# Kernel tuning notes

Hardware: AMD Instinct MI355X
Metric: run time of the kernel (lower is better)

The kernel has to match this reference:

```python
import jax, jax.numpy as jnp
import numpy as np

B, S, D_MODEL, N_HEADS, HIDDEN = 4, 2048, 1024, 16, 4096
D_HEAD = D_MODEL // N_HEADS
LN_EPS = 1e-5


def setup_inputs() -> dict:
    key = jax.random.key(0)
    ks = jax.random.split(key, 20)
    s = 0.02
    return {
        "X": jax.random.normal(ks[0], (B, S, D_MODEL), dtype=jnp.float32),
        # attention projections (stored [in, out]; y = x @ W + b)
        "Wq": jax.random.normal(ks[1], (D_MODEL, D_MODEL), dtype=jnp.float32) * s,
        "bq": jnp.zeros((D_MODEL,), jnp.float32),
        "Wk": jax.random.normal(ks[2], (D_MODEL, D_MODEL), dtype=jnp.float32) * s,
        "bk": jnp.zeros((D_MODEL,), jnp.float32),
        "Wv": jax.random.normal(ks[3], (D_MODEL, D_MODEL), dtype=jnp.float32) * s,
        "bv": jnp.zeros((D_MODEL,), jnp.float32),
        "Wo": jax.random.normal(ks[4], (D_MODEL, D_MODEL), dtype=jnp.float32) * s,
        "bo": jnp.zeros((D_MODEL,), jnp.float32),
        # layernorm 1
        "g1": jnp.ones((D_MODEL,), jnp.float32),
        "beta1": jnp.zeros((D_MODEL,), jnp.float32),
        # FFN
        "W1": jax.random.normal(ks[5], (D_MODEL, HIDDEN), dtype=jnp.float32) * s,
        "b1": jnp.zeros((HIDDEN,), jnp.float32),
        "W2": jax.random.normal(ks[6], (HIDDEN, D_MODEL), dtype=jnp.float32) * s,
        "b2": jnp.zeros((D_MODEL,), jnp.float32),
        # layernorm 2
        "g2": jnp.ones((D_MODEL,), jnp.float32),
        "beta2": jnp.zeros((D_MODEL,), jnp.float32),
    }


def _layer_norm(x, gamma, beta):
    mu = jnp.mean(x, axis=-1, keepdims=True)
    var = jnp.mean(jnp.square(x - mu), axis=-1, keepdims=True)
    return (x - mu) * jax.lax.rsqrt(var + LN_EPS) * gamma + beta


def reference(X, Wq, bq, Wk, bk, Wv, bv, Wo, bo, g1, beta1, W1, b1, W2, b2, g2, beta2):
    b, s, d = X.shape
    # multi-head attention (dropout is identity in eval mode)
    q = (X @ Wq + bq).reshape(b, s, N_HEADS, D_HEAD)
    k = (X @ Wk + bk).reshape(b, s, N_HEADS, D_HEAD)
    v = (X @ Wv + bv).reshape(b, s, N_HEADS, D_HEAD)
    scale = 1.0 / np.sqrt(D_HEAD).astype(np.float32)
    scores = jnp.einsum('bqhd,bkhd->bhqk', q, k) * scale
    attn = jax.nn.softmax(scores, axis=-1)
    ctx = jnp.einsum('bhqk,bkhd->bqhd', attn, v).reshape(b, s, d)
    attn_out = ctx @ Wo + bo
    # AddNorm 1
    Y = _layer_norm(X + attn_out, g1, beta1)
    # FFN
    ffn_out = jax.nn.relu(Y @ W1 + b1) @ W2 + b2
    # AddNorm 2
    return _layer_norm(Y + ffn_out, g2, beta2)
```

## Files before the change

### kernel.cpp

```cpp
#include <hip/hip_runtime.h>
#include <stdint.h>

typedef unsigned short u16;
typedef short bf16x8 __attribute__((ext_vector_type(8)));
typedef float f32x4 __attribute__((ext_vector_type(4)));
typedef float f32x16 __attribute__((ext_vector_type(16)));
typedef u16 u16x4 __attribute__((ext_vector_type(4)));
typedef u16 u16x8 __attribute__((ext_vector_type(8)));

#define LOG2E 1.4426950408889634f
#define QSCALE (0.125f * LOG2E)

__device__ __forceinline__ u16 f2bf(float f) {
  union { float f; uint32_t u; } x; x.f = f;
  uint32_t r = x.u + 0x7fffu + ((x.u >> 16) & 1u);
  return (u16)(r >> 16);
}
__device__ __forceinline__ u16 f2bf_ru(float f) {
  union { float f; uint32_t u; } x; x.f = f;
  return (u16)((x.u + 0x8000u) >> 16);
}
__device__ __forceinline__ float bf2f(u16 h) {
  union { uint32_t u; float f; } x; x.u = ((uint32_t)h) << 16;
  return x.f;
}
__device__ __forceinline__ uint32_t cvtpk(float lo, float hi) {
  uint32_t r;
  asm("v_cvt_pk_bf16_f32 %0, %1, %2" : "=v"(r) : "v"(lo), "v"(hi));
  return r;
}
__device__ __forceinline__ int swz3(int row) { return (row ^ (row >> 3)) & 7; }

__device__ __forceinline__ void gload_lds16(const void* g, void* lds) {
  __builtin_amdgcn_global_load_lds(
      (const __attribute__((address_space(1))) void*)g,
      (__attribute__((address_space(3))) void*)lds, 16, 0, 0);
}

__global__ __launch_bounds__(256) void cast_bf16(const float* __restrict__ in,
                                                 u16* __restrict__ out, int n8) {
  int i = blockIdx.x * 256 + threadIdx.x;
  const int stride = gridDim.x * 256;
  for (; i < n8; i += stride) {
    const f32x4* p = (const f32x4*)in + (size_t)i * 2;
    f32x4 a = p[0], b = p[1];
    u16x8 o;
    o[0] = f2bf(a[0]); o[1] = f2bf(a[1]); o[2] = f2bf(a[2]); o[3] = f2bf(a[3]);
    o[4] = f2bf(b[0]); o[5] = f2bf(b[1]); o[6] = f2bf(b[2]); o[7] = f2bf(b[3]);
    ((u16x8*)out)[i] = o;
  }
}

__global__ __launch_bounds__(256) void concat3(const float* __restrict__ a,
                                               const float* __restrict__ b,
                                               const float* __restrict__ c,
                                               float* __restrict__ o) {
  int i = blockIdx.x * 256 + threadIdx.x;
  if (i < 3072)
    o[i] = i < 1024 ? a[i] * QSCALE : (i < 2048 ? b[i - 1024] : c[i - 2048]);
}

__global__ __launch_bounds__(256) void transpose_cast(const float* __restrict__ in,
                                                      u16* __restrict__ out, int R, int C,
                                                      float scale) {
  __shared__ float tile[32][33];
  const int bc = blockIdx.x * 32, br = blockIdx.y * 32;
  const int tx = threadIdx.x & 31, ty = threadIdx.x >> 5;
#pragma unroll
  for (int i = 0; i < 32; i += 8)
    tile[ty + i][tx] = in[(size_t)(br + ty + i) * C + bc + tx];
  __syncthreads();
#pragma unroll
  for (int i = 0; i < 32; i += 8)
    out[(size_t)(bc + ty + i) * R + br + tx] = f2bf(tile[tx][ty + i] * scale);
}

__global__ __launch_bounds__(256) void vtrans(const u16* __restrict__ QKV,
                                              u16* __restrict__ Vtg) {
  __shared__ u16 tl[64][65];
  const int t = threadIdx.x;
  const int sblk = blockIdx.x, h = blockIdx.y, b = blockIdx.z;
  const int s0 = sblk * 64;
  const size_t ibase = ((size_t)b * 2048) * 3072 + 2048 + h * 64;
#pragma unroll
  for (int i = 0; i < 2; i++) {
    const int idx = i * 256 + t;
    const int sl = idx >> 3, d0 = (idx & 7) * 8;
    bf16x8 v = *(const bf16x8*)&QKV[ibase + (size_t)(s0 + sl) * 3072 + d0];
#pragma unroll
    for (int e = 0; e < 8; e++) tl[d0 + e][sl] = (u16)v[e];
  }
  __syncthreads();
  const size_t ob = ((size_t)(b * 16 + h) * 64) * 2048;
#pragma unroll
  for (int i = 0; i < 2; i++) {
    const int idx = i * 256 + t;
    const int r = idx >> 3, c0 = (idx & 7) * 8;
    u16x8 o;
#pragma unroll
    for (int e = 0; e < 8; e++) o[e] = tl[r][c0 + e];
    *(u16x8*)&Vtg[ob + (size_t)r * 2048 + s0 + c0] = o;
  }
}

template <int RELU>
__global__ __launch_bounds__(256) void gemm_bt(const u16* __restrict__ A,
                                               const u16* __restrict__ BT,
                                               const float* __restrict__ bias,
                                               u16* __restrict__ Cb,
                                               int M, int N, int K) {
  constexpr int BM = 128, BN = 128, BK = 64;
  __shared__ u16 As[BM * BK];
  __shared__ u16 Bs[BN * BK];
  const int t = threadIdx.x;
  const int w = t >> 6, lane = t & 63;
  const int la = lane & 15, lb = lane >> 4;
  const int wr = w >> 1, wc = w & 1;
  const int m0 = blockIdx.y * BM, n0 = blockIdx.x * BN;

  f32x4 acc[4][4];
#pragma unroll
  for (int i = 0; i < 4; i++)
#pragma unroll
    for (int j = 0; j < 4; j++) acc[i][j] = (f32x4){0.f, 0.f, 0.f, 0.f};

  for (int kt = 0; kt < K; kt += BK) {
#pragma unroll
    for (int i = 0; i < 4; i++) {
      const int s = i * 256 + t;
      const int row = s >> 3, col = (s & 7) * 8;
      gload_lds16(A + (size_t)(m0 + row) * K + kt + col, &As[(i * 256 + w * 64) * 8]);
      gload_lds16(BT + (size_t)(n0 + row) * K + kt + col, &Bs[(i * 256 + w * 64) * 8]);
    }
    __syncthreads();
#pragma unroll
    for (int ks = 0; ks < 2; ks++) {
      bf16x8 af[4], bfr[4];
#pragma unroll
      for (int i = 0; i < 4; i++)
        af[i] = *(const bf16x8*)&As[(wr * 64 + i * 16 + la) * BK + ks * 32 + lb * 8];
#pragma unroll
      for (int j = 0; j < 4; j++)
        bfr[j] = *(const bf16x8*)&Bs[(wc * 64 + j * 16 + la) * BK + ks * 32 + lb * 8];
#pragma unroll
      for (int i = 0; i < 4; i++)
#pragma unroll
        for (int j = 0; j < 4; j++)
          acc[i][j] = __builtin_amdgcn_mfma_f32_16x16x32_bf16(af[i], bfr[j], acc[i][j], 0, 0, 0);
    }
    __syncthreads();
  }
#pragma unroll
  for (int i = 0; i < 4; i++) {
    const int r = m0 + wr * 64 + i * 16 + lb * 4;
#pragma unroll
    for (int j = 0; j < 4; j++) {
      const int c = n0 + wc * 64 + j * 16 + la;
      const float bv = bias[c];
#pragma unroll
      for (int rr = 0; rr < 4; rr++) {
        float v = acc[i][j][rr] + bv;
        if (RELU) v = fmaxf(v, 0.f);
        Cb[(size_t)(r + rr) * N + c] = f2bf(v);
      }
    }
  }
}

template <int RELU>
__global__ __launch_bounds__(512, 2) void gemm8p(const u16* __restrict__ A,
                                                 const u16* __restrict__ BT,
                                                 const float* __restrict__ bias,
                                                 u16* __restrict__ Cb,
                                                 int M, int N, int K, int nbx) {
  __shared__ u16 As[2][256 * 64];
  __shared__ u16 Bs[2][256 * 64];
  const int t = threadIdx.x;
  const int w = t >> 6, lane = t & 63;
  const int la = lane & 15, lb = lane >> 4;
  const int wr = w >> 2, wc = w & 3;
  int bid = (int)blockIdx.x;
  const int cpx = (int)gridDim.x >> 3;
  bid = (bid & 7) * cpx + (bid >> 3);
  const int m0 = (bid / nbx) * 256, n0 = (bid % nbx) * 256;
  const int NT = K >> 6;
  const int row64 = t >> 3;
  const int colp = ((t & 7) ^ swz3(row64)) << 3;

#define STG_A(buf, tile, q) \
  gload_lds16(A + (size_t)(m0 + (q)*64 + row64) * K + ((tile) << 6) + colp, \
              &As[buf][(q)*4096 + w * 512])
#define STG_B(buf, tile, q) \
  gload_lds16(BT + (size_t)(n0 + (q)*64 + row64) * K + ((tile) << 6) + colp, \
              &Bs[buf][(q)*4096 + w * 512])
#define LDA(dst, mf, ks) { const int r_ = wr * 128 + (mf)*16 + la; \
  dst = *(const bf16x8*)&As[cur][r_ * 64 + (((((ks) << 2) + lb) ^ swz3(r_)) << 3)]; }
#define LDB(dst, nf, ks) { const int r_ = wc * 64 + (nf)*16 + la; \
  dst = *(const bf16x8*)&Bs[cur][r_ * 64 + (((((ks) << 2) + lb) ^ swz3(r_)) << 3)]; }
#define MFMA16(mh, nh, barr) \
  __builtin_amdgcn_s_setprio(1); \
  _Pragma("unroll") for (int ks = 0; ks < 2; ks++) \
  _Pragma("unroll") for (int i = 0; i < 4; i++) \
  _Pragma("unroll") for (int j = 0; j < 2; j++) \
    acc[(mh)*4 + i][(nh)*2 + j] = __builtin_amdgcn_mfma_f32_16x16x32_bf16( \
        af[i][ks], barr[j][ks], acc[(mh)*4 + i][(nh)*2 + j], 0, 0, 0); \
  __builtin_amdgcn_s_setprio(0);
#define BAR1() __builtin_amdgcn_s_barrier(); \
  asm volatile("s_waitcnt lgkmcnt(0)" ::: "memory"); \
  __builtin_amdgcn_sched_barrier(0)

  f32x4 acc[8][4];
#pragma unroll
  for (int i = 0; i < 8; i++)
#pragma unroll
    for (int j = 0; j < 4; j++) acc[i][j] = (f32x4){0.f, 0.f, 0.f, 0.f};

  STG_A(0, 0, 0); STG_A(0, 0, 2);
  STG_B(0, 0, 0); STG_B(0, 0, 1); STG_B(0, 0, 2); STG_B(0, 0, 3);
  STG_A(0, 0, 1); STG_A(0, 0, 3);
  asm volatile("s_waitcnt vmcnt(2)" ::: "memory");
  __builtin_amdgcn_s_barrier();

  for (int tile = 0; tile < NT; ++tile) {
    const int cur = tile & 1, nxt = cur ^ 1;
    const bool hn = (tile + 1) < NT;
    bf16x8 af[4][2], b0[2][2], b1[2][2];
#pragma unroll
    for (int i = 0; i < 4; i++) { LDA(af[i][0], i, 0); LDA(af[i][1], i, 1); }
#pragma unroll
    for (int j = 0; j < 2; j++) { LDB(b0[j][0], j, 0); LDB(b0[j][1], j, 1); }
    if (hn) { STG_A(nxt, tile + 1, 0); STG_A(nxt, tile + 1, 2); }
    BAR1();
    MFMA16(0, 0, b0);
    __builtin_amdgcn_s_barrier();
#pragma unroll
    for (int j = 0; j < 2; j++) { LDB(b1[j][0], 2 + j, 0); LDB(b1[j][1], 2 + j, 1); }
    if (hn) { STG_B(nxt, tile + 1, 0); STG_B(nxt, tile + 1, 1); }
    BAR1();
    MFMA16(0, 1, b1);
    if (hn) { asm volatile("s_waitcnt vmcnt(4)" ::: "memory"); }
    else    { asm volatile("s_waitcnt vmcnt(0)" ::: "memory"); }
    __builtin_amdgcn_s_barrier();
#pragma unroll
    for (int i = 0; i < 4; i++) { LDA(af[i][0], 4 + i, 0); LDA(af[i][1], 4 + i, 1); }
    if (hn) { STG_B(nxt, tile + 1, 2); STG_B(nxt, tile + 1, 3); }
    BAR1();
    MFMA16(1, 0, b0);
    __builtin_amdgcn_s_barrier();
    if (hn) { STG_A(nxt, tile + 1, 1); STG_A(nxt, tile + 1, 3); }
    BAR1();
    MFMA16(1, 1, b1);
    if (hn) { asm volatile("s_waitcnt vmcnt(2)" ::: "memory"); }
    __builtin_amdgcn_s_barrier();
  }
#undef STG_A
#undef STG_B
#undef LDA
#undef LDB
#undef MFMA16
#undef BAR1

#pragma unroll
  for (int mf = 0; mf < 8; mf++) {
    const int r = m0 + wr * 128 + mf * 16 + lb * 4;
#pragma unroll
    for (int nf = 0; nf < 4; nf++) {
      const int c = n0 + wc * 64 + nf * 16 + la;
      const float bv = bias[c];
#pragma unroll
      for (int rr = 0; rr < 4; rr++) {
        float v = acc[mf][nf][rr] + bv;
        if (RELU) v = fmaxf(v, 0.f);
        Cb[(size_t)(r + rr) * N + c] = f2bf(v);
      }
    }
  }
}

template <int RELU>
__global__ __launch_bounds__(512, 2) void gemm8n(const u16* __restrict__ A,
                                                 const u16* __restrict__ BT,
                                                 const float* __restrict__ bias,
                                                 u16* __restrict__ Cb,
                                                 int M, int N, int K, int nbx) {
  __shared__ u16 As[2][128 * 64];
  __shared__ u16 Bs[2][256 * 64];
  const int t = threadIdx.x;
  const int w = t >> 6, lane = t & 63;
  const int la = lane & 15, lb = lane >> 4;
  const int wr = w >> 2, wc = w & 3;
  int bid = (int)blockIdx.x;
  const int cpx = (int)gridDim.x >> 3;
  bid = (bid & 7) * cpx + (bid >> 3);
  const int m0 = (bid / nbx) * 128, n0 = (bid % nbx) * 256;
  const int NT = K >> 6;
  const int rowA = t >> 3;
  const int colpA = ((t & 7) ^ swz3(rowA)) << 3;

#define STG_An(buf, tile, q) \
  gload_lds16(A + (size_t)(m0 + (q)*64 + rowA) * K + ((tile) << 6) + colpA, \
              &As[buf][(q)*4096 + t * 8])
#define STG_Bn(buf, tile, c, i) { \
  const int r32_ = (i)*64 + (t >> 3); \
  const int R_ = ((r32_ >> 5) << 6) + (c)*32 + (r32_ & 31); \
  const int cp_ = ((t & 7) ^ swz3(R_)) << 3; \
  gload_lds16(BT + (size_t)(n0 + R_) * K + ((tile) << 6) + cp_, \
              &Bs[buf][R_ * 64 + (t & 7) * 8]); }
#define LDAn(dst, mf, ks) { const int r_ = wr * 64 + (mf)*16 + la; \
  dst = *(const bf16x8*)&As[cur][r_ * 64 + (((((ks) << 2) + lb) ^ swz3(r_)) << 3)]; }
#define LDBn(dst, nf, ks) { const int r_ = wc * 64 + (nf)*16 + la; \
  dst = *(const bf16x8*)&Bs[cur][r_ * 64 + (((((ks) << 2) + lb) ^ swz3(r_)) << 3)]; }
#define MFMAn(nh, barr) \
  __builtin_amdgcn_s_setprio(1); \
  _Pragma("unroll") for (int ks = 0; ks < 2; ks++) \
  _Pragma("unroll") for (int i = 0; i < 4; i++) \
  _Pragma("unroll") for (int j = 0; j < 2; j++) \
    acc[i][(nh)*2 + j] = __builtin_amdgcn_mfma_f32_16x16x32_bf16( \
        af[i][ks], barr[j][ks], acc[i][(nh)*2 + j], 0, 0, 0); \
  __builtin_amdgcn_s_setprio(0);
#define BARn() __builtin_amdgcn_s_barrier(); \
  asm volatile("s_waitcnt lgkmcnt(0)" ::: "memory"); \
  __builtin_amdgcn_sched_barrier(0)

  f32x4 acc[4][4];
#pragma unroll
  for (int i = 0; i < 4; i++)
#pragma unroll
    for (int j = 0; j < 4; j++) acc[i][j] = (f32x4){0.f, 0.f, 0.f, 0.f};

  STG_Bn(0, 0, 0, 0); STG_Bn(0, 0, 0, 1); STG_An(0, 0, 0);
  STG_An(0, 0, 1); STG_Bn(0, 0, 1, 0); STG_Bn(0, 0, 1, 1);
  asm volatile("s_waitcnt vmcnt(0)" ::: "memory");
  __builtin_amdgcn_s_barrier();

  for (int tile = 0; tile < NT; ++tile) {
    const int cur = tile & 1, nxt = cur ^ 1;
    const bool hn = (tile + 1) < NT;
    bf16x8 af[4][2], b0[2][2], b1[2][2];
#pragma unroll
    for (int i = 0; i < 4; i++) { LDAn(af[i][0], i, 0); LDAn(af[i][1], i, 1); }
#pragma unroll
    for (int j = 0; j < 2; j++) { LDBn(b0[j][0], j, 0); LDBn(b0[j][1], j, 1); }
    if (hn) { STG_Bn(nxt, tile + 1, 0, 0); STG_Bn(nxt, tile + 1, 0, 1); STG_An(nxt, tile + 1, 0); }
    BARn();
    MFMAn(0, b0);
    if (hn) { asm volatile("s_waitcnt vmcnt(3)" ::: "memory"); }
    else    { asm volatile("s_waitcnt vmcnt(0)" ::: "memory"); }
    __builtin_amdgcn_s_barrier();
#pragma unroll
    for (int j = 0; j < 2; j++) { LDBn(b1[j][0], 2 + j, 0); LDBn(b1[j][1], 2 + j, 1); }
    if (hn) { STG_An(nxt, tile + 1, 1); STG_Bn(nxt, tile + 1, 1, 0); STG_Bn(nxt, tile + 1, 1, 1); }
    BARn();
    MFMAn(1, b1);
    if (hn) { asm volatile("s_waitcnt vmcnt(2)" ::: "memory"); }
    __builtin_amdgcn_s_barrier();
  }
#undef STG_An
#undef STG_Bn
#undef LDAn
#undef LDBn
#undef MFMAn
#undef BARn

#pragma unroll
  for (int mf = 0; mf < 4; mf++) {
    const int r = m0 + wr * 64 + mf * 16 + lb * 4;
#pragma unroll
    for (int nf = 0; nf < 4; nf++) {
      const int c = n0 + wc * 64 + nf * 16 + la;
      const float bv = bias[c];
#pragma unroll
      for (int rr = 0; rr < 4; rr++) {
        float v = acc[mf][nf][rr] + bv;
        if (RELU) v = fmaxf(v, 0.f);
        Cb[(size_t)(r + rr) * N + c] = f2bf(v);
      }
    }
  }
}

__global__ __launch_bounds__(256, 3) void attn_fwd(const u16* __restrict__ Qg,
                                                   const u16* __restrict__ Kg,
                                                   const u16* __restrict__ Vtg,
                                                   u16* __restrict__ Og, int LDM) {
  constexpr int S = 2048, DMO = 1024, NT = S / 64;
  __shared__ u16 Ks[2][64 * 64];
  __shared__ u16 Vt[2][64 * 64];
  const int t = threadIdx.x, w = t >> 6, lane = t & 63;
  const int l5 = lane & 31, hf = lane >> 5;
  const int qb = blockIdx.x, h = blockIdx.y, b = blockIdx.z;
  const size_t base = ((size_t)b * S) * LDM + h * 64;
  const size_t vbase = ((size_t)(b * 16 + h) * 64) * 2048;
  const size_t obase = ((size_t)b * S) * DMO + h * 64;
  const int qrow0 = qb * 128 + w * 32;

#define ATT_STAGE(buf, kt_) { \
  _Pragma("unroll") for (int i = 0; i < 2; i++) { \
    const int s = i * 256 + t; const int r = s >> 3; const int cg = s & 7; \
    gload_lds16(Kg + base + (size_t)((kt_) + r) * LDM + ((cg ^ swz3(r)) << 3), \
                &Ks[buf][s * 8]); } \
  _Pragma("unroll") for (int i = 0; i < 2; i++) { \
    const int s = i * 256 + t; const int r = s >> 3; const int cg = s & 7; \
    gload_lds16(Vtg + vbase + (size_t)r * 2048 + (kt_) + ((cg ^ swz3(r)) << 3), \
                &Vt[buf][s * 8]); } }

  bf16x8 qf[4];
#pragma unroll
  for (int kb = 0; kb < 4; kb++)
    qf[kb] = *(const bf16x8*)&Qg[base + (size_t)(qrow0 + l5) * LDM + kb * 16 + hf * 8];

  f32x16 accO0, accO1, accL;
#pragma unroll
  for (int i = 0; i < 16; i++) { accO0[i] = 0.f; accO1[i] = 0.f; accL[i] = 0.f; }
  float m = -1e30f;

  bf16x8 ones;
#pragma unroll
  for (int i = 0; i < 8; i++) ones[i] = (short)0x3F80;

  ATT_STAGE(0, 0);
  asm volatile("s_waitcnt vmcnt(0)" ::: "memory");
  __builtin_amdgcn_s_barrier();

  for (int kt = 0; kt < NT; ++kt) {
    const int cur = kt & 1;
    if (kt + 1 < NT) ATT_STAGE(cur ^ 1, (kt + 1) * 64);

    f32x16 st0, st1;
#pragma unroll
    for (int i = 0; i < 16; i++) { st0[i] = 0.f; st1[i] = 0.f; }
    __builtin_amdgcn_s_setprio(1);
#pragma unroll
    for (int kb = 0; kb < 4; kb++) {
      const int r0 = l5, r1 = 32 + l5;
      bf16x8 kf0 = *(const bf16x8*)&Ks[cur][r0 * 64 + (((hf + 2 * kb) ^ swz3(r0)) << 3)];
      bf16x8 kf1 = *(const bf16x8*)&Ks[cur][r1 * 64 + (((hf + 2 * kb) ^ swz3(r1)) << 3)];
      st0 = __builtin_amdgcn_mfma_f32_32x32x16_bf16(kf0, qf[kb], st0, 0, 0, 0);
      st1 = __builtin_amdgcn_mfma_f32_32x32x16_bf16(kf1, qf[kb], st1, 0, 0, 0);
    }
    __builtin_amdgcn_s_setprio(0);

    float rm = st0[0];
#pragma unroll
    for (int i = 1; i < 16; i++) rm = fmaxf(rm, st0[i]);
#pragma unroll
    for (int i = 0; i < 16; i++) rm = fmaxf(rm, st1[i]);
    if (__any(rm > m + 8.0f)) {
      float ra = rm, rb = rm;
      asm volatile("v_permlane32_swap_b32 %0, %1" : "+v"(ra), "+v"(rb));
      rm = fmaxf(rm, fmaxf(ra, rb));
      const float mN = fmaxf(m, rm);
      const float al = exp2f(m - mN);
      m = mN;
#pragma unroll
      for (int r = 0; r < 16; r++) {
        const float alr = __shfl(al, (r & 3) + 8 * (r >> 2) + 4 * hf, 64);
        accO0[r] *= alr; accO1[r] *= alr; accL[r] *= alr;
      }
    }

    uint32_t pw0[8], pw1[8];
#pragma unroll
    for (int r2 = 0; r2 < 8; r2++) {
      pw0[r2] = cvtpk(exp2f(st0[2 * r2] - m), exp2f(st0[2 * r2 + 1] - m));
      pw1[r2] = cvtpk(exp2f(st1[2 * r2] - m), exp2f(st1[2 * r2 + 1] - m));
    }
    bf16x8 pf[4];
    {
      uint32_t a0 = pw0[0], b0v = pw0[2], a1 = pw0[1], b1v = pw0[3];
      asm volatile("v_permlane32_swap_b32 %0, %1" : "+v"(a0), "+v"(b0v));
      asm volatile("v_permlane32_swap_b32 %0, %1" : "+v"(a1), "+v"(b1v));
      union { uint32_t u[4]; bf16x8 v; } k;
      k.u[0] = a0; k.u[1] = a1; k.u[2] = b0v; k.u[3] = b1v; pf[0] = k.v;
      uint32_t c0 = pw0[4], d0 = pw0[6], c1 = pw0[5], d1 = pw0[7];
      asm volatile("v_permlane32_swap_b32 %0, %1" : "+v"(c0), "+v"(d0));
      asm volatile("v_permlane32_swap_b32 %0, %1" : "+v"(c1), "+v"(d1));
      k.u[0] = c0; k.u[1] = c1; k.u[2] = d0; k.u[3] = d1; pf[1] = k.v;
      uint32_t e0 = pw1[0], f0 = pw1[2], e1 = pw1[1], f1 = pw1[3];
      asm volatile("v_permlane32_swap_b32 %0, %1" : "+v"(e0), "+v"(f0));
      asm volatile("v_permlane32_swap_b32 %0, %1" : "+v"(e1), "+v"(f1));
      k.u[0] = e0; k.u[1] = e1; k.u[2] = f0; k.u[3] = f1; pf[2] = k.v;
      uint32_t g0 = pw1[4], h0 = pw1[6], g1 = pw1[5], h1 = pw1[7];
      asm volatile("v_permlane32_swap_b32 %0, %1" : "+v"(g0), "+v"(h0));
      asm volatile("v_permlane32_swap_b32 %0, %1" : "+v"(g1), "+v"(h1));
      k.u[0] = g0; k.u[1] = g1; k.u[2] = h0; k.u[3] = h1; pf[3] = k.v;
    }

    __builtin_amdgcn_s_setprio(1);
#pragma unroll
    for (int kb = 0; kb < 4; kb++) {
      const int r0 = l5, r1 = 32 + l5;
      bf16x8 vf0 = *(const bf16x8*)&Vt[cur][r0 * 64 + (((hf + 2 * kb) ^ swz3(r0)) << 3)];
      bf16x8 vf1 = *(const bf16x8*)&Vt[cur][r1 * 64 + (((hf + 2 * kb) ^ swz3(r1)) << 3)];
      accO0 = __builtin_amdgcn_mfma_f32_32x32x16_bf16(pf[kb], vf0, accO0, 0, 0, 0);
      accO1 = __builtin_amdgcn_mfma_f32_32x32x16_bf16(pf[kb], vf1, accO1, 0, 0, 0);
      accL  = __builtin_amdgcn_mfma_f32_32x32x16_bf16(pf[kb], ones, accL, 0, 0, 0);
    }
    __builtin_amdgcn_s_setprio(0);

    asm volatile("s_waitcnt vmcnt(0)" ::: "memory");
    __builtin_amdgcn_s_barrier();
  }
#undef ATT_STAGE

#pragma unroll
  for (int r = 0; r < 16; r++) {
    const float inv = 1.0f / accL[r];
    const int row = qrow0 + (r & 3) + 8 * (r >> 2) + 4 * hf;
    Og[obase + (size_t)row * DMO + l5]      = f2bf_ru(accO0[r] * inv);
    Og[obase + (size_t)row * DMO + 32 + l5] = f2bf_ru(accO1[r] * inv);
  }
}

template <int AF32, int OUTF32>
__global__ __launch_bounds__(256) void add_ln(const void* __restrict__ Ap,
                                              const u16* __restrict__ Bb,
                                              const float* __restrict__ g,
                                              const float* __restrict__ be,
                                              void* __restrict__ Yp) {
  constexpr int D = 1024;
  const int row = blockIdx.x, t = threadIdx.x;
  f32x4 a;
  if (AF32) {
    a = ((const f32x4*)((const float*)Ap + (size_t)row * D))[t];
  } else {
    u16x4 av = ((const u16x4*)((const u16*)Ap + (size_t)row * D))[t];
#pragma unroll
    for (int i = 0; i < 4; i++) a[i] = bf2f(av[i]);
  }
  u16x4 bv16 = ((const u16x4*)(Bb + (size_t)row * D))[t];
  f32x4 x;
#pragma unroll
  for (int i = 0; i < 4; i++) x[i] = a[i] + bf2f(bv16[i]);
  float s1 = x[0] + x[1] + x[2] + x[3];
  float s2 = x[0] * x[0] + x[1] * x[1] + x[2] * x[2] + x[3] * x[3];
#pragma unroll
  for (int off = 32; off > 0; off >>= 1) {
    s1 += __shfl_down(s1, off, 64);
    s2 += __shfl_down(s2, off, 64);
  }
  __shared__ float sm[8];
  const int w = t >> 6, lane = t & 63;
  if (lane == 0) { sm[w] = s1; sm[4 + w] = s2; }
  __syncthreads();
  s1 = sm[0] + sm[1] + sm[2] + sm[3];
  s2 = sm[4] + sm[5] + sm[6] + sm[7];
  const float mean = s1 * (1.0f / D);
  const float var = s2 * (1.0f / D) - mean * mean;
  const float rstd = rsqrtf(var + 1e-5f);
  const f32x4 gv = ((const f32x4*)g)[t];
  const f32x4 bv = ((const f32x4*)be)[t];
  f32x4 y;
#pragma unroll
  for (int i = 0; i < 4; i++) y[i] = (x[i] - mean) * rstd * gv[i] + bv[i];
  if (OUTF32) {
    ((f32x4*)((float*)Yp + (size_t)row * D))[t] = y;
  } else {
    u16x4 o;
#pragma unroll
    for (int i = 0; i < 4; i++) o[i] = f2bf(y[i]);
    ((u16x4*)((u16*)Yp + (size_t)row * D))[t] = o;
  }
}

extern "C" void kernel_launch(void* const* d_in, const int* in_sizes, int n_in,
                              void* d_out, int out_size, void* d_ws, size_t ws_size,
                              hipStream_t stream) {
  const float* X   = (const float*)d_in[0];
  const float* Wq  = (const float*)d_in[1];
  const float* bq  = (const float*)d_in[2];
  const float* Wk  = (const float*)d_in[3];
  const float* bk  = (const float*)d_in[4];
  const float* Wv  = (const float*)d_in[5];
  const float* bv  = (const float*)d_in[6];
  const float* Wo  = (const float*)d_in[7];
  const float* bo  = (const float*)d_in[8];
  const float* g1  = (const float*)d_in[9];
  const float* be1 = (const float*)d_in[10];
  const float* W1  = (const float*)d_in[11];
  const float* b1  = (const float*)d_in[12];
  const float* W2  = (const float*)d_in[13];
  const float* b2  = (const float*)d_in[14];
  const float* g2  = (const float*)d_in[15];
  const float* be2 = (const float*)d_in[16];

  const size_t MB = 1ull << 20;
  char* wsb = (char*)d_ws;
  u16*   WqkvT = (u16*)(wsb + 0 * MB);
  u16*   WoT   = (u16*)(wsb + 6 * MB);
  u16*   W1T   = (u16*)(wsb + 8 * MB);
  u16*   W2T   = (u16*)(wsb + 16 * MB);
  u16*   Xb    = (u16*)(wsb + 24 * MB);
  u16*   Ab    = (u16*)(wsb + 24 * MB);
  u16*   Fb    = (u16*)(wsb + 24 * MB);
  u16*   QKVb  = (u16*)(wsb + 40 * MB);
  u16*   Hb    = (u16*)(wsb + 40 * MB);
  float* bqkv  = (float*)(wsb + 88 * MB);
  u16*   Cx    = (u16*)(wsb + 88 * MB);
  u16*   Vt_g  = (u16*)(wsb + 104 * MB);
  u16*   Yb    = (u16*)(wsb + 104 * MB);
  (void)ws_size; (void)in_sizes; (void)n_in; (void)out_size;

  cast_bf16<<<2048, 256, 0, stream>>>(X, Xb, 8192 * 1024 / 8);
  concat3<<<12, 256, 0, stream>>>(bq, bk, bv, bqkv);
  transpose_cast<<<dim3(32, 32), 256, 0, stream>>>(Wq, WqkvT, 1024, 1024, QSCALE);
  transpose_cast<<<dim3(32, 32), 256, 0, stream>>>(Wk, WqkvT + 1024 * 1024, 1024, 1024, 1.0f);
  transpose_cast<<<dim3(32, 32), 256, 0, stream>>>(Wv, WqkvT + 2 * 1024 * 1024, 1024, 1024, 1.0f);
  transpose_cast<<<dim3(32, 32), 256, 0, stream>>>(Wo, WoT, 1024, 1024, 1.0f);
  transpose_cast<<<dim3(128, 32), 256, 0, stream>>>(W1, W1T, 1024, 4096, 1.0f);
  transpose_cast<<<dim3(32, 128), 256, 0, stream>>>(W2, W2T, 4096, 1024, 1.0f);

  gemm8p<0><<<384, 512, 0, stream>>>(Xb, WqkvT, bqkv, QKVb, 8192, 3072, 1024, 12);

  vtrans<<<dim3(32, 16, 4), 256, 0, stream>>>(QKVb, Vt_g);
  attn_fwd<<<dim3(16, 16, 4), 256, 0, stream>>>(QKVb, QKVb + 1024, Vt_g, Cx, 3072);

  gemm8n<0><<<256, 512, 0, stream>>>(Cx, WoT, bo, Ab, 8192, 1024, 1024, 4);
  add_ln<1, 0><<<8192, 256, 0, stream>>>(X, Ab, g1, be1, Yb);
  gemm8p<1><<<512, 512, 0, stream>>>(Yb, W1T, b1, Hb, 8192, 4096, 1024, 16);
  gemm8n<0><<<256, 512, 0, stream>>>(Hb, W2T, b2, Fb, 8192, 1024, 4096, 4);
  add_ln<0, 1><<<8192, 256, 0, stream>>>(Yb, Fb, g2, be2, d_out);
}
```

Measured before the change: 442.1 us.

## Switch gemm8p to 32x32x16 MFMA and tree-reduce attention row max

New measurement: 430.9 us (median of 5 runs). 1.03x faster.

```diff
diff --git a/kernel.cpp b/kernel.cpp
--- a/kernel.cpp
+++ b/kernel.cpp
@@ -104,70 +104,6 @@
 }
 
 template <int RELU>
-__global__ __launch_bounds__(256) void gemm_bt(const u16* __restrict__ A,
-                                               const u16* __restrict__ BT,
-                                               const float* __restrict__ bias,
-                                               u16* __restrict__ Cb,
-                                               int M, int N, int K) {
-  constexpr int BM = 128, BN = 128, BK = 64;
-  __shared__ u16 As[BM * BK];
-  __shared__ u16 Bs[BN * BK];
-  const int t = threadIdx.x;
-  const int w = t >> 6, lane = t & 63;
-  const int la = lane & 15, lb = lane >> 4;
-  const int wr = w >> 1, wc = w & 1;
-  const int m0 = blockIdx.y * BM, n0 = blockIdx.x * BN;
-
-  f32x4 acc[4][4];
-#pragma unroll
-  for (int i = 0; i < 4; i++)
-#pragma unroll
-    for (int j = 0; j < 4; j++) acc[i][j] = (f32x4){0.f, 0.f, 0.f, 0.f};
-
-  for (int kt = 0; kt < K; kt += BK) {
-#pragma unroll
-    for (int i = 0; i < 4; i++) {
-      const int s = i * 256 + t;
-      const int row = s >> 3, col = (s & 7) * 8;
-      gload_lds16(A + (size_t)(m0 + row) * K + kt + col, &As[(i * 256 + w * 64) * 8]);
-      gload_lds16(BT + (size_t)(n0 + row) * K + kt + col, &Bs[(i * 256 + w * 64) * 8]);
-    }
-    __syncthreads();
-#pragma unroll
-    for (int ks = 0; ks < 2; ks++) {
-      bf16x8 af[4], bfr[4];
-#pragma unroll
-      for (int i = 0; i < 4; i++)
-        af[i] = *(const bf16x8*)&As[(wr * 64 + i * 16 + la) * BK + ks * 32 + lb * 8];
-#pragma unroll
-      for (int j = 0; j < 4; j++)
-        bfr[j] = *(const bf16x8*)&Bs[(wc * 64 + j * 16 + la) * BK + ks * 32 + lb * 8];
-#pragma unroll
-      for (int i = 0; i < 4; i++)
-#pragma unroll
-        for (int j = 0; j < 4; j++)
-          acc[i][j] = __builtin_amdgcn_mfma_f32_16x16x32_bf16(af[i], bfr[j], acc[i][j], 0, 0, 0);
-    }
-    __syncthreads();
-  }
-#pragma unroll
-  for (int i = 0; i < 4; i++) {
-    const int r = m0 + wr * 64 + i * 16 + lb * 4;
-#pragma unroll
-    for (int j = 0; j < 4; j++) {
-      const int c = n0 + wc * 64 + j * 16 + la;
-      const float bv = bias[c];
-#pragma unroll
-      for (int rr = 0; rr < 4; rr++) {
-        float v = acc[i][j][rr] + bv;
-        if (RELU) v = fmaxf(v, 0.f);
-        Cb[(size_t)(r + rr) * N + c] = f2bf(v);
-      }
-    }
-  }
-}
-
-template <int RELU>
 __global__ __launch_bounds__(512, 2) void gemm8p(const u16* __restrict__ A,
                                                  const u16* __restrict__ BT,
                                                  const float* __restrict__ bias,
@@ -177,7 +113,7 @@
   __shared__ u16 Bs[2][256 * 64];
   const int t = threadIdx.x;
   const int w = t >> 6, lane = t & 63;
-  const int la = lane & 15, lb = lane >> 4;
+  const int l5 = lane & 31, hf = lane >> 5;
   const int wr = w >> 2, wc = w & 3;
   int bid = (int)blockIdx.x;
   const int cpx = (int)gridDim.x >> 3;
@@ -193,27 +129,26 @@
 #define STG_B(buf, tile, q) \
   gload_lds16(BT + (size_t)(n0 + (q)*64 + row64) * K + ((tile) << 6) + colp, \
               &Bs[buf][(q)*4096 + w * 512])
-#define LDA(dst, mf, ks) { const int r_ = wr * 128 + (mf)*16 + la; \
-  dst = *(const bf16x8*)&As[cur][r_ * 64 + (((((ks) << 2) + lb) ^ swz3(r_)) << 3)]; }
-#define LDB(dst, nf, ks) { const int r_ = wc * 64 + (nf)*16 + la; \
-  dst = *(const bf16x8*)&Bs[cur][r_ * 64 + (((((ks) << 2) + lb) ^ swz3(r_)) << 3)]; }
-#define MFMA16(mh, nh, barr) \
+#define LDA32(dst, mfi, kb) { const int r_ = wr * 128 + (mfi)*32 + l5; \
+  dst = *(const bf16x8*)&As[cur][r_ * 64 + (((((kb) << 1) + hf) ^ swz3(r_)) << 3)]; }
+#define LDB32(dst, nfi, kb) { const int r_ = wc * 64 + (nfi)*32 + l5; \
+  dst = *(const bf16x8*)&Bs[cur][r_ * 64 + (((((kb) << 1) + hf) ^ swz3(r_)) << 3)]; }
+#define MFMA32(mh, nfi, barr) \
   __builtin_amdgcn_s_setprio(1); \
-  _Pragma("unroll") for (int ks = 0; ks < 2; ks++) \
-  _Pragma("unroll") for (int i = 0; i < 4; i++) \
-  _Pragma("unroll") for (int j = 0; j < 2; j++) \
-    acc[(mh)*4 + i][(nh)*2 + j] = __builtin_amdgcn_mfma_f32_16x16x32_bf16( \
-        af[i][ks], barr[j][ks], acc[(mh)*4 + i][(nh)*2 + j], 0, 0, 0); \
+  _Pragma("unroll") for (int kb = 0; kb < 4; kb++) \
+  _Pragma("unroll") for (int i = 0; i < 2; i++) \
+    acc[((mh)*2 + i) * 2 + (nfi)] = __builtin_amdgcn_mfma_f32_32x32x16_bf16( \
+        af[i][kb], barr[kb], acc[((mh)*2 + i) * 2 + (nfi)], 0, 0, 0); \
   __builtin_amdgcn_s_setprio(0);
 #define BAR1() __builtin_amdgcn_s_barrier(); \
   asm volatile("s_waitcnt lgkmcnt(0)" ::: "memory"); \
   __builtin_amdgcn_sched_barrier(0)
 
-  f32x4 acc[8][4];
+  f32x16 acc[8];
 #pragma unroll
   for (int i = 0; i < 8; i++)
 #pragma unroll
-    for (int j = 0; j < 4; j++) acc[i][j] = (f32x4){0.f, 0.f, 0.f, 0.f};
+    for (int j = 0; j < 16; j++) acc[i][j] = 0.f;
 
   STG_A(0, 0, 0); STG_A(0, 0, 2);
   STG_B(0, 0, 0); STG_B(0, 0, 1); STG_B(0, 0, 2); STG_B(0, 0, 3);
@@ -224,54 +159,54 @@
   for (int tile = 0; tile < NT; ++tile) {
     const int cur = tile & 1, nxt = cur ^ 1;
     const bool hn = (tile + 1) < NT;
-    bf16x8 af[4][2], b0[2][2], b1[2][2];
-#pragma unroll
-    for (int i = 0; i < 4; i++) { LDA(af[i][0], i, 0); LDA(af[i][1], i, 1); }
-#pragma unroll
-    for (int j = 0; j < 2; j++) { LDB(b0[j][0], j, 0); LDB(b0[j][1], j, 1); }
+    bf16x8 af[2][4], b0[4], b1[4];
+#pragma unroll
+    for (int kb = 0; kb < 4; kb++) { LDA32(af[0][kb], 0, kb); LDA32(af[1][kb], 1, kb); }
+#pragma unroll
+    for (int kb = 0; kb < 4; kb++) { LDB32(b0[kb], 0, kb); }
     if (hn) { STG_A(nxt, tile + 1, 0); STG_A(nxt, tile + 1, 2); }
     BAR1();
-    MFMA16(0, 0, b0);
-    __builtin_amdgcn_s_barrier();
-#pragma unroll
-    for (int j = 0; j < 2; j++) { LDB(b1[j][0], 2 + j, 0); LDB(b1[j][1], 2 + j, 1); }
+    MFMA32(0, 0, b0);
+    __builtin_amdgcn_s_barrier();
+#pragma unroll
+    for (int kb = 0; kb < 4; kb++) { LDB32(b1[kb], 1, kb); }
     if (hn) { STG_B(nxt, tile + 1, 0); STG_B(nxt, tile + 1, 1); }
     BAR1();
-    MFMA16(0, 1, b1);
+    MFMA32(0, 1, b1);
     if (hn) { asm volatile("s_waitcnt vmcnt(4)" ::: "memory"); }
     else    { asm volatile("s_waitcnt vmcnt(0)" ::: "memory"); }
     __builtin_amdgcn_s_barrier();
 #pragma unroll
-    for (int i = 0; i < 4; i++) { LDA(af[i][0], 4 + i, 0); LDA(af[i][1], 4 + i, 1); }
+    for (int kb = 0; kb < 4; kb++) { LDA32(af[0][kb], 2, kb); LDA32(af[1][kb], 3, kb); }
     if (hn) { STG_B(nxt, tile + 1, 2); STG_B(nxt, tile + 1, 3); }
     BAR1();
-    MFMA16(1, 0, b0);
+    MFMA32(1, 0, b0);
     __builtin_amdgcn_s_barrier();
     if (hn) { STG_A(nxt, tile + 1, 1); STG_A(nxt, tile + 1, 3); }
     BAR1();
-    MFMA16(1, 1, b1);
+    MFMA32(1, 1, b1);
     if (hn) { asm volatile("s_waitcnt vmcnt(2)" ::: "memory"); }
     __builtin_amdgcn_s_barrier();
   }
 #undef STG_A
 #undef STG_B
-#undef LDA
-#undef LDB
-#undef MFMA16
+#undef LDA32
+#undef LDB32
+#undef MFMA32
 #undef BAR1
 
 #pragma unroll
-  for (int mf = 0; mf < 8; mf++) {
-    const int r = m0 + wr * 128 + mf * 16 + lb * 4;
-#pragma unroll
-    for (int nf = 0; nf < 4; nf++) {
-      const int c = n0 + wc * 64 + nf * 16 + la;
+  for (int mf = 0; mf < 4; mf++) {
+#pragma unroll
+    for (int nf = 0; nf < 2; nf++) {
+      const int c = n0 + wc * 64 + nf * 32 + l5;
       const float bv = bias[c];
 #pragma unroll
-      for (int rr = 0; rr < 4; rr++) {
-        float v = acc[mf][nf][rr] + bv;
+      for (int reg = 0; reg < 16; reg++) {
+        const int r = m0 + wr * 128 + mf * 32 + (reg & 3) + 8 * (reg >> 2) + 4 * hf;
+        float v = acc[mf * 2 + nf][reg] + bv;
         if (RELU) v = fmaxf(v, 0.f);
-        Cb[(size_t)(r + rr) * N + c] = f2bf(v);
+        Cb[(size_t)r * N + c] = f2bf(v);
       }
     }
   }
@@ -440,11 +375,18 @@
     }
     __builtin_amdgcn_s_setprio(0);
 
-    float rm = st0[0];
-#pragma unroll
-    for (int i = 1; i < 16; i++) rm = fmaxf(rm, st0[i]);
-#pragma unroll
-    for (int i = 0; i < 16; i++) rm = fmaxf(rm, st1[i]);
+    float tm[16];
+#pragma unroll
+    for (int i = 0; i < 8; i++) tm[i] = fmaxf(st0[2 * i], st0[2 * i + 1]);
+#pragma unroll
+    for (int i = 0; i < 8; i++) tm[8 + i] = fmaxf(st1[2 * i], st1[2 * i + 1]);
+#pragma unroll
+    for (int i = 0; i < 8; i++) tm[i] = fmaxf(tm[i], tm[i + 8]);
+#pragma unroll
+    for (int i = 0; i < 4; i++) tm[i] = fmaxf(tm[i], tm[i + 4]);
+    tm[0] = fmaxf(tm[0], tm[2]);
+    tm[1] = fmaxf(tm[1], tm[3]);
+    float rm = fmaxf(tm[0], tm[1]);
     if (__any(rm > m + 8.0f)) {
       float ra = rm, rb = rm;
       asm volatile("v_permlane32_swap_b32 %0, %1" : "+v"(ra), "+v"(rb));
```
